# Kernel optimization log

Measured on AMD Instinct MI355X. Metric: run time of the kernel, lower is better.

## Reference

```python
import jax, jax.numpy as jnp
import numpy as np

NUM_HEADS = 8
NUM_POINTS = 4            # sampling points per pillar point
NUM_PILLAR = 4            # points in pillar
SAMPLING_RADIUS = 0.12


def masked_softmax(logits, mask):
    # logits/mask: [B, N, H, P]; softmax over last dim, robust to fully-masked rows
    m = mask.astype(logits.dtype)
    w = jax.nn.softmax(jnp.where(mask, logits, jnp.asarray(-1e9, logits.dtype)), axis=-1) * m
    return w / jnp.clip(jnp.sum(w, axis=-1, keepdims=True), 1e-6)


def grid_sample_bilinear(feat, loc):
    # feat: [G, D, H, W]; loc: [G, Nq, P, 2] normalized to [0,1]
    # matches torch grid_sample(mode='bilinear', padding_mode='zeros', align_corners=False)
    G, D, H, W = feat.shape
    _, Nq, P, _ = loc.shape
    fm = feat.reshape(G, D, H * W).transpose(0, 2, 1)  # [G, HW, D]
    x = loc[..., 0] * W - 0.5
    y = loc[..., 1] * H - 0.5
    x0 = jnp.floor(x)
    y0 = jnp.floor(y)
    wx = x - x0
    wy = y - y0
    out = jnp.zeros((G, Nq * P, D), dtype=feat.dtype)
    corners = [(0, 0, (1 - wx) * (1 - wy)), (1, 0, wx * (1 - wy)),
               (0, 1, (1 - wx) * wy), (1, 1, wx * wy)]
    for dx, dy, w in corners:
        xi = x0 + dx
        yi = y0 + dy
        valid = (xi >= 0) & (xi < W) & (yi >= 0) & (yi < H)
        xc = jnp.clip(xi, 0, W - 1).astype(jnp.int32)
        yc = jnp.clip(yi, 0, H - 1).astype(jnp.int32)
        idx = (yc * W + xc).reshape(G, Nq * P)
        g = jnp.take_along_axis(fm, idx[:, :, None], axis=1)  # [G, Nq*P, D]
        out = out + g * (w * valid.astype(feat.dtype)).reshape(G, Nq * P, 1)
    return out.reshape(G, Nq, P, D)


def setup_inputs() -> dict:
    key = jax.random.key(0)
    ks = jax.random.split(key, 10)
    B, N, C = 1, 10000, 256
    n_cams, Himg, Wimg = 6, 60, 100
    HD = NUM_HEADS * NUM_PILLAR * NUM_POINTS  # 128
    query = jax.random.normal(ks[0], (B, N, C), jnp.float32)
    image_feats = jax.random.normal(ks[1], (B, n_cams, C, Himg, Wimg), jnp.float32)
    reference_points_cam = jax.random.uniform(ks[2], (B, n_cams, N, NUM_PILLAR, 2), jnp.float32)
    bev_mask = jax.random.bernoulli(ks[3], 0.4, (B, n_cams, N, NUM_PILLAR))
    s = 0.02
    offset_W = jax.random.normal(ks[4], (C, HD * 2), jnp.float32) * s
    offset_b = jnp.zeros((HD * 2,), jnp.float32)
    weight_W = jax.random.normal(ks[5], (C, HD), jnp.float32) * s
    weight_b = jnp.zeros((HD,), jnp.float32)
    out_W = jax.random.normal(ks[6], (C, C), jnp.float32) * s
    out_b = jnp.zeros((C,), jnp.float32)
    return {"query": query, "image_feats": image_feats,
            "reference_points_cam": reference_points_cam, "bev_mask": bev_mask,
            "offset_W": offset_W, "offset_b": offset_b,
            "weight_W": weight_W, "weight_b": weight_b,
            "out_W": out_W, "out_b": out_b}


def reference(query, image_feats, reference_points_cam, bev_mask,
              offset_W, offset_b, weight_W, weight_b, out_W, out_b):
    B, N, C = query.shape
    _, n_cams, _, Himg, Wimg = image_feats.shape
    Hh, Pp, Pn = NUM_HEADS, NUM_PILLAR, NUM_POINTS
    P = Pp * Pn
    hd = C // Hh

    offsets = jnp.tanh(query @ offset_W + offset_b) * SAMPLING_RADIUS
    offsets = offsets.reshape(B, N, Hh, Pp, Pn, 2)
    weight_logits = (query @ weight_W + weight_b).reshape(B, N, Hh, P)

    fused = jnp.zeros((B, N, C), query.dtype)
    counts = jnp.zeros((B, N), jnp.int32)
    for cam in range(n_cams):
        ref = reference_points_cam[:, cam]          # [B, N, Pp, 2]
        visible = bev_mask[:, cam]                  # [B, N, Pp]
        loc = ref[:, :, None, :, None, :] + offsets  # [B, N, H, Pp, Pn, 2]
        loc = loc.reshape(B, N, Hh, P, 2)
        vmask = jnp.broadcast_to(visible[:, :, None, :, None], (B, N, Hh, Pp, Pn)).reshape(B, N, Hh, P)
        w = masked_softmax(weight_logits, vmask)    # [B, N, H, P]
        feat = image_feats[:, cam].reshape(B * Hh, hd, Himg, Wimg)
        grid = loc.transpose(0, 2, 1, 3, 4).reshape(B * Hh, N, P, 2)
        samp = grid_sample_bilinear(feat, grid)     # [B*H, N, P, hd]
        samp = samp.reshape(B, Hh, N, P, hd).transpose(0, 2, 1, 3, 4)  # [B, N, H, P, hd]
        cam_out = jnp.sum(samp * w[..., None], axis=3).reshape(B, N, C)
        has_vis = jnp.any(visible, axis=-1)         # [B, N]
        fused = fused + cam_out * has_vis[..., None].astype(cam_out.dtype)
        counts = counts + has_vis.astype(jnp.int32)
    fused = fused / jnp.clip(counts, 1)[..., None].astype(fused.dtype)
    return fused @ out_W + out_b
```

## Files before the change

kernel.cpp:

```cpp
#include <hip/hip_runtime.h>
#include <hip/hip_bf16.h>

#define N_Q   10000
#define N_CAM 6
#define HIMG  60
#define WIMG  100
#define NPIX  6000

typedef __attribute__((ext_vector_type(4))) float f32x4;
typedef __attribute__((ext_vector_type(2))) float f32x2;
typedef __attribute__((ext_vector_type(8))) short bf16x8;

__device__ __forceinline__ unsigned short f2bf(float x) {
  __hip_bfloat16 b = __float2bfloat16(x);
  return *reinterpret_cast<unsigned short*>(&b);
}
__device__ __forceinline__ float bf2f(unsigned short u) {
  return __uint_as_float(((unsigned)u) << 16);
}
__device__ __forceinline__ float bf16lo(unsigned int u) {
  return __uint_as_float(u << 16);
}
__device__ __forceinline__ float bf16hi(unsigned int u) {
  return __uint_as_float(u & 0xffff0000u);
}
__device__ __forceinline__ void pk_fma(f32x2& acc, f32x2 a, f32x2 b) {
  asm("v_pk_fma_f32 %0, %1, %2, %0" : "+v"(acc) : "v"(a), "v"(b));
}
__device__ __forceinline__ void split8(const float* pa, bf16x8& ah, bf16x8& al) {
  const float4 v0 = *reinterpret_cast<const float4*>(pa);
  const float4 v1 = *reinterpret_cast<const float4*>(pa + 4);
  const float v[8] = {v0.x, v0.y, v0.z, v0.w, v1.x, v1.y, v1.z, v1.w};
#pragma unroll
  for (int j = 0; j < 8; ++j) {
    const unsigned short hb = f2bf(v[j]);
    ah[j] = (short)hb;
    al[j] = (short)f2bf(v[j] - bf2f(hb));
  }
}

__global__ __launch_bounds__(256) void wprep_k(
    const float* __restrict__ oW, const float* __restrict__ wW,
    const float* __restrict__ outW,
    unsigned short* __restrict__ oWth,  unsigned short* __restrict__ oWtl,
    unsigned short* __restrict__ wWth,  unsigned short* __restrict__ wWtl,
    unsigned short* __restrict__ outWth,unsigned short* __restrict__ outWtl) {
  const int b = blockIdx.x, k = threadIdx.x;
  float v; unsigned short *dh, *dl; int idx;
  if (b < 256) {
    v = oW[k * 256 + b]; dh = oWth; dl = oWtl; idx = b * 256 + k;
  } else if (b < 384) {
    int nn = b - 256; v = wW[k * 128 + nn]; dh = wWth; dl = wWtl; idx = nn * 256 + k;
  } else {
    int nn = b - 384; v = outW[k * 256 + nn]; dh = outWth; dl = outWtl; idx = nn * 256 + k;
  }
  unsigned short hv = f2bf(v);
  dh[idx] = hv;
  dl[idx] = f2bf(v - bf2f(hv));
}

__device__ __forceinline__ void gemm_bodyA32(
    const float* __restrict__ A,
    const unsigned short* __restrict__ Bh, const unsigned short* __restrict__ Bl,
    const float* __restrict__ bias, float* __restrict__ C,
    int M, int N, int mode, int bm, int bn, int tid) {
  const int l = tid & 63, w = tid >> 6;
  const int wm = w >> 1, wn = w & 1;
  const int lr = l & 15;
  const int lk = (l >> 4) * 8;

  const int am0 = min(bm + wm * 32 + lr, M - 1);
  const int am1 = min(bm + wm * 32 + 16 + lr, M - 1);
  const int bn0 = bn + wn * 32 + lr;
  const int bn1 = bn0 + 16;

  const float* pa0 = A + (size_t)am0 * 256 + lk;
  const float* pa1 = A + (size_t)am1 * 256 + lk;
  const bf16x8* pbh0 = (const bf16x8*)(Bh + (size_t)bn0 * 256 + lk);
  const bf16x8* pbh1 = (const bf16x8*)(Bh + (size_t)bn1 * 256 + lk);
  const bf16x8* pbl0 = (const bf16x8*)(Bl + (size_t)bn0 * 256 + lk);
  const bf16x8* pbl1 = (const bf16x8*)(Bl + (size_t)bn1 * 256 + lk);

  f32x4 acc00 = {}, acc01 = {}, acc10 = {}, acc11 = {};

#pragma unroll
  for (int ks = 0; ks < 8; ++ks) {
    bf16x8 ah0, al0, ah1, al1;
    split8(pa0 + ks * 32, ah0, al0);
    split8(pa1 + ks * 32, ah1, al1);
    bf16x8 bh0 = pbh0[ks * 4], bh1 = pbh1[ks * 4];
    bf16x8 bl0 = pbl0[ks * 4], bl1 = pbl1[ks * 4];
    acc00 = __builtin_amdgcn_mfma_f32_16x16x32_bf16(ah0, bh0, acc00, 0, 0, 0);
    acc00 = __builtin_amdgcn_mfma_f32_16x16x32_bf16(ah0, bl0, acc00, 0, 0, 0);
    acc00 = __builtin_amdgcn_mfma_f32_16x16x32_bf16(al0, bh0, acc00, 0, 0, 0);
    acc01 = __builtin_amdgcn_mfma_f32_16x16x32_bf16(ah0, bh1, acc01, 0, 0, 0);
    acc01 = __builtin_amdgcn_mfma_f32_16x16x32_bf16(ah0, bl1, acc01, 0, 0, 0);
    acc01 = __builtin_amdgcn_mfma_f32_16x16x32_bf16(al0, bh1, acc01, 0, 0, 0);
    acc10 = __builtin_amdgcn_mfma_f32_16x16x32_bf16(ah1, bh0, acc10, 0, 0, 0);
    acc10 = __builtin_amdgcn_mfma_f32_16x16x32_bf16(ah1, bl0, acc10, 0, 0, 0);
    acc10 = __builtin_amdgcn_mfma_f32_16x16x32_bf16(al1, bh0, acc10, 0, 0, 0);
    acc11 = __builtin_amdgcn_mfma_f32_16x16x32_bf16(ah1, bh1, acc11, 0, 0, 0);
    acc11 = __builtin_amdgcn_mfma_f32_16x16x32_bf16(ah1, bl1, acc11, 0, 0, 0);
    acc11 = __builtin_amdgcn_mfma_f32_16x16x32_bf16(al1, bh1, acc11, 0, 0, 0);
  }

  const float bias0 = bias[bn + wn * 32 + lr];
  const float bias1 = bias[bn + wn * 32 + 16 + lr];
  const int row0 = bm + wm * 32 + (l >> 4) * 4;
  const int col0 = bn + wn * 32 + lr;
#pragma unroll
  for (int r = 0; r < 4; ++r) {
    int rowA = row0 + r, rowB = row0 + 16 + r;
    float v00 = acc00[r] + bias0, v01 = acc01[r] + bias1;
    float v10 = acc10[r] + bias0, v11 = acc11[r] + bias1;
    if (mode == 1) {
      v00 = tanhf(v00) * 0.12f; v01 = tanhf(v01) * 0.12f;
      v10 = tanhf(v10) * 0.12f; v11 = tanhf(v11) * 0.12f;
    } else if (mode == 2) {
      v00 = __expf(v00); v01 = __expf(v01);
      v10 = __expf(v10); v11 = __expf(v11);
    }
    if (rowA < M) {
      C[(size_t)rowA * N + col0] = v00;
      C[(size_t)rowA * N + col0 + 16] = v01;
    }
    if (rowB < M) {
      C[(size_t)rowB * N + col0] = v10;
      C[(size_t)rowB * N + col0 + 16] = v11;
    }
  }
}

#define TRANS_BLKS (N_CAM * 94)
#define G12_BLKS   (157 * 6)

__global__ __launch_bounds__(256) void fused_prep_gemm_k(
    const float* __restrict__ in,
    const float* __restrict__ q,
    unsigned short* __restrict__ ftout,
    const unsigned short* __restrict__ B1h, const unsigned short* __restrict__ B1l,
    const float* __restrict__ b1, float* __restrict__ C1,
    const unsigned short* __restrict__ B2h, const unsigned short* __restrict__ B2l,
    const float* __restrict__ b2, float* __restrict__ C2) {
  __shared__ float tile[64][65];
  const int tid = threadIdx.x;
  if (blockIdx.x < TRANS_BLKS) {
    const int cam = blockIdx.x / 94;
    const int px0 = (blockIdx.x % 94) * 64;
    const int lpx = tid & 63;
    const int cg  = tid >> 6;
    const int px  = px0 + lpx;
    const bool pv = px < NPIX;

    for (int c0 = 0; c0 < 256; c0 += 64) {
#pragma unroll
      for (int i = 0; i < 16; ++i) {
        int cc = cg * 16 + i;
        tile[lpx][cc] = pv ? in[(cam * 256 + c0 + cc) * NPIX + px] : 0.f;
      }
      __syncthreads();
      const int wc = tid & 63;
      const int pg = tid >> 6;
#pragma unroll
      for (int i = 0; i < 16; ++i) {
        int lp = pg * 16 + i;
        int gpx = px0 + lp;
        if (gpx < NPIX)
          ftout[(size_t)(cam * NPIX + gpx) * 256 + c0 + wc] = f2bf(tile[lp][wc]);
      }
      __syncthreads();
    }
    return;
  }
  const int b  = blockIdx.x - TRANS_BLKS;
  const int bt = b % 6;
  const int bm = (b / 6) * 64;
  if (bt < 4)
    gemm_bodyA32(q, B1h, B1l, b1, C1, N_Q, 256, 1, bm, bt * 64, tid);
  else
    gemm_bodyA32(q, B2h, B2l, b2, C2, N_Q, 128, 2, bm, (bt - 4) * 64, tid);
}

__global__ __launch_bounds__(256) void sample_cam(
    const unsigned short* __restrict__ ft,
    const float* __restrict__ offs,
    const float* __restrict__ wlog,
    const float* __restrict__ refp,
    const int*   __restrict__ mask,
    unsigned short* __restrict__ partial) {
  const int tid = threadIdx.x;
  const int sub = tid >> 7;
  const int t   = tid & 127;
  const int cam = blockIdx.x / (N_Q / 2);
  const int n   = (blockIdx.x % (N_Q / 2)) * 2 + sub;
  const int h   = t >> 4;
  const int p   = t & 15;
  const int pp  = p >> 2;
  const int c   = (t >> 2) & 3;
  const int ch  = t & 3;

  const int vis = mask[(cam * N_Q + n) * 4 + pp];
  const unsigned long long bal = __ballot(vis != 0);
  if (!(bal & 0x1111ULL)) return;

  __shared__ float spt[2][1216];
  float* lds = spt[sub];
  unsigned int* ldsu = reinterpret_cast<unsigned int*>(lds);

  const float2 off = reinterpret_cast<const float2*>(offs)[n * 128 + t];
  const float E = wlog[n * 128 + t];
  const uint4* ftq2 = reinterpret_cast<const uint4*>(ft)
                      + (size_t)cam * (NPIX * 32) + (unsigned)(h * 4 + ch);

  const int abase = h * 152 + p * 9;
  const int rbase = h * 152;

  float e = vis ? E : 0.f;
  float s = e;
#pragma unroll
  for (int m = 8; m >= 1; m >>= 1)
    s += __shfl_xor(s, m, 16);
  const float wgt = e / fmaxf(s, 1e-6f);

  const float2 ref = reinterpret_cast<const float2*>(refp)[(cam * N_Q + n) * 4 + pp];
  const float x = fmaf(ref.x + off.x, (float)WIMG, -0.5f);
  const float y = fmaf(ref.y + off.y, (float)HIMG, -0.5f);
  const float x0f = floorf(x), y0f = floorf(y);
  const float wx = x - x0f, wy = y - y0f;
  const int x0 = (int)x0f, y0 = (int)y0f;
  const int x1 = x0 + 1, y1 = y0 + 1;
  const float mx0 = (x0 >= 0 && x0 < WIMG) ? 1.f : 0.f;
  const float mx1 = (x1 >= 0 && x1 < WIMG) ? 1.f : 0.f;
  const float my0 = (y0 >= 0 && y0 < HIMG) ? 1.f : 0.f;
  const float my1 = (y1 >= 0 && y1 < HIMG) ? 1.f : 0.f;
  const int xc0 = min(max(x0, 0), WIMG - 1);
  const int xc1 = min(max(x1, 0), WIMG - 1);
  const int yc0 = min(max(y0, 0), HIMG - 1);
  const int yc1 = min(max(y1, 0), HIMG - 1);
  lds[abase + 0] = (1.f - wx) * (1.f - wy) * mx0 * my0 * wgt;
  lds[abase + 1] = wx * (1.f - wy) * mx1 * my0 * wgt;
  lds[abase + 2] = (1.f - wx) * wy * mx0 * my1 * wgt;
  lds[abase + 3] = wx * wy * mx1 * my1 * wgt;
  ldsu[abase + 4] = (unsigned)(yc0 * WIMG + xc0);
  ldsu[abase + 5] = (unsigned)(yc0 * WIMG + xc1);
  ldsu[abase + 6] = (unsigned)(yc1 * WIMG + xc0);
  ldsu[abase + 7] = (unsigned)(yc1 * WIMG + xc1);
  __builtin_amdgcn_wave_barrier();

  f32x2 acc2[4] = {{0.f, 0.f}, {0.f, 0.f}, {0.f, 0.f}, {0.f, 0.f}};
  const bool pv0 = (bal      ) & 1ULL;
  const bool pv1 = (bal >>  4) & 1ULL;
  const bool pv2 = (bal >>  8) & 1ULL;
  const bool pv3 = (bal >> 12) & 1ULL;
  uint4 u0[4], u1[4], u2[4], u3[4];

#define ISSUE(U, P)                                                          \
  if (pv##P) {                                                               \
    _Pragma("unroll")                                                        \
    for (int pn = 0; pn < 4; ++pn) {                                         \
      const unsigned pix = ldsu[rbase + ((P) * 4 + pn) * 9 + 4 + c];         \
      U[pn] = ftq2[pix * 32u];                                               \
    }                                                                        \
  }
  ISSUE(u0, 0) ISSUE(u1, 1) ISSUE(u2, 2) ISSUE(u3, 3)

#define CONSUME(U, P)                                                        \
  if (pv##P) {                                                               \
    _Pragma("unroll")                                                        \
    for (int pn = 0; pn < 4; ++pn) {                                         \
      const float wv = lds[rbase + ((P) * 4 + pn) * 9 + c];                  \
      const f32x2 w2 = {wv, wv};                                             \
      f32x2 a;                                                               \
      a.x = bf16lo(U[pn].x); a.y = __uint_as_float(U[pn].x);                 \
      pk_fma(acc2[0], a, w2);                                                \
      a.x = bf16lo(U[pn].y); a.y = __uint_as_float(U[pn].y);                 \
      pk_fma(acc2[1], a, w2);                                                \
      a.x = bf16lo(U[pn].z); a.y = __uint_as_float(U[pn].z);                 \
      pk_fma(acc2[2], a, w2);                                                \
      a.x = bf16lo(U[pn].w); a.y = __uint_as_float(U[pn].w);                 \
      pk_fma(acc2[3], a, w2);                                                \
    }                                                                        \
  }
  CONSUME(u0, 0) CONSUME(u1, 1) CONSUME(u2, 2) CONSUME(u3, 3)
#undef ISSUE
#undef CONSUME

  float acc[8];
#pragma unroll
  for (int j = 0; j < 4; ++j) { acc[2 * j] = acc2[j].x; acc[2 * j + 1] = acc2[j].y; }
#pragma unroll
  for (int j = 0; j < 8; ++j) acc[j] += __shfl_xor(acc[j], 4);
#pragma unroll
  for (int j = 0; j < 8; ++j) acc[j] += __shfl_xor(acc[j], 8);

  if (c == 0) {
    unsigned w01 = (unsigned)f2bf(acc[0]) | ((unsigned)f2bf(acc[1]) << 16);
    unsigned w23 = (unsigned)f2bf(acc[2]) | ((unsigned)f2bf(acc[3]) << 16);
    unsigned w45 = (unsigned)f2bf(acc[4]) | ((unsigned)f2bf(acc[5]) << 16);
    unsigned w67 = (unsigned)f2bf(acc[6]) | ((unsigned)f2bf(acc[7]) << 16);
    uint4 v = {w01, w23, w45, w67};
    reinterpret_cast<uint4*>(partial)[((size_t)cam * N_Q + n) * 32 + h * 4 + ch] = v;
  }
}

__global__ __launch_bounds__(256) void combine_k(
    const unsigned short* __restrict__ partial,
    const int*   __restrict__ mask,
    unsigned short* __restrict__ fh,
    unsigned short* __restrict__ fl) {
  const int tid  = threadIdx.x;
  const int sub  = tid >> 6;
  const int lane = tid & 63;
  const int n    = blockIdx.x * 4 + sub;

  __shared__ int sv[4][6];
  if (tid < 24) {
    const int qi = tid / 6, cam = tid - qi * 6;
    const int nn = blockIdx.x * 4 + qi;
    const int4 m4 = *reinterpret_cast<const int4*>(&mask[(cam * N_Q + nn) * 4]);
    sv[qi][cam] = (m4.x | m4.y | m4.z | m4.w) ? 1 : 0;
  }
  __syncthreads();

  f32x4 s4 = {0.f, 0.f, 0.f, 0.f};
  int cnt = 0;
#pragma unroll
  for (int cam = 0; cam < N_CAM; ++cam) {
    if (sv[sub][cam]) {
      const uint2 v = reinterpret_cast<const uint2*>(partial)
                          [((size_t)cam * N_Q + n) * 64 + lane];
      s4[0] += bf16lo(v.x); s4[1] += bf16hi(v.x);
      s4[2] += bf16lo(v.y); s4[3] += bf16hi(v.y);
      cnt++;
    }
  }
  const float inv = (cnt > 0) ? (1.f / (float)cnt) : 1.f;
  unsigned short hs[4], ls[4];
#pragma unroll
  for (int j = 0; j < 4; ++j) {
    const float v = s4[j] * inv;
    hs[j] = f2bf(v);
    ls[j] = f2bf(v - bf2f(hs[j]));
  }
  uint2 vh = {(unsigned)hs[0] | ((unsigned)hs[1] << 16),
              (unsigned)hs[2] | ((unsigned)hs[3] << 16)};
  uint2 vl = {(unsigned)ls[0] | ((unsigned)ls[1] << 16),
              (unsigned)ls[2] | ((unsigned)ls[3] << 16)};
  reinterpret_cast<uint2*>(fh)[n * 64 + lane] = vh;
  reinterpret_cast<uint2*>(fl)[n * 64 + lane] = vl;
}

__global__ __launch_bounds__(256) void gemm_out_k(
    const unsigned short* __restrict__ Ah, const unsigned short* __restrict__ Al,
    const unsigned short* __restrict__ Bh, const unsigned short* __restrict__ Bl,
    const float* __restrict__ bias, float* __restrict__ C) {
  const int tid = threadIdx.x;
  const int l = tid & 63, w = tid >> 6;
  const int wm = w >> 1, wn = w & 1;
  const int bm = blockIdx.y * 64, bn = blockIdx.x * 64;
  const int lr = l & 15;
  const int lk = (l >> 4) * 8;
  const int M = N_Q, N = 256;

  const int am0 = min(bm + wm * 32 + lr, M - 1);
  const int am1 = min(bm + wm * 32 + 16 + lr, M - 1);
  const int bn0 = bn + wn * 32 + lr;
  const int bn1 = bn0 + 16;

  const bf16x8* pah0 = (const bf16x8*)(Ah + (size_t)am0 * 256 + lk);
  const bf16x8* pah1 = (const bf16x8*)(Ah + (size_t)am1 * 256 + lk);
  const bf16x8* pal0 = (const bf16x8*)(Al + (size_t)am0 * 256 + lk);
  const bf16x8* pal1 = (const bf16x8*)(Al + (size_t)am1 * 256 + lk);
  const bf16x8* pbh0 = (const bf16x8*)(Bh + (size_t)bn0 * 256 + lk);
  const bf16x8* pbh1 = (const bf16x8*)(Bh + (size_t)bn1 * 256 + lk);
  const bf16x8* pbl0 = (const bf16x8*)(Bl + (size_t)bn0 * 256 + lk);
  const bf16x8* pbl1 = (const bf16x8*)(Bl + (size_t)bn1 * 256 + lk);

  f32x4 acc00 = {}, acc01 = {}, acc10 = {}, acc11 = {};

#pragma unroll
  for (int ks = 0; ks < 8; ++ks) {
    bf16x8 ah0 = pah0[ks * 4], ah1 = pah1[ks * 4];
    bf16x8 al0 = pal0[ks * 4], al1 = pal1[ks * 4];
    bf16x8 bh0 = pbh0[ks * 4], bh1 = pbh1[ks * 4];
    bf16x8 bl0 = pbl0[ks * 4], bl1 = pbl1[ks * 4];
    acc00 = __builtin_amdgcn_mfma_f32_16x16x32_bf16(ah0, bh0, acc00, 0, 0, 0);
    acc00 = __builtin_amdgcn_mfma_f32_16x16x32_bf16(ah0, bl0, acc00, 0, 0, 0);
    acc00 = __builtin_amdgcn_mfma_f32_16x16x32_bf16(al0, bh0, acc00, 0, 0, 0);
    acc01 = __builtin_amdgcn_mfma_f32_16x16x32_bf16(ah0, bh1, acc01, 0, 0, 0);
    acc01 = __builtin_amdgcn_mfma_f32_16x16x32_bf16(ah0, bl1, acc01, 0, 0, 0);
    acc01 = __builtin_amdgcn_mfma_f32_16x16x32_bf16(al0, bh1, acc01, 0, 0, 0);
    acc10 = __builtin_amdgcn_mfma_f32_16x16x32_bf16(ah1, bh0, acc10, 0, 0, 0);
    acc10 = __builtin_amdgcn_mfma_f32_16x16x32_bf16(ah1, bl0, acc10, 0, 0, 0);
    acc10 = __builtin_amdgcn_mfma_f32_16x16x32_bf16(al1, bh0, acc10, 0, 0, 0);
    acc11 = __builtin_amdgcn_mfma_f32_16x16x32_bf16(ah1, bh1, acc11, 0, 0, 0);
    acc11 = __builtin_amdgcn_mfma_f32_16x16x32_bf16(ah1, bl1, acc11, 0, 0, 0);
    acc11 = __builtin_amdgcn_mfma_f32_16x16x32_bf16(al1, bh1, acc11, 0, 0, 0);
  }

  const float bias0 = bias[bn + wn * 32 + lr];
  const float bias1 = bias[bn + wn * 32 + 16 + lr];
  const int row0 = bm + wm * 32 + (l >> 4) * 4;
  const int col0 = bn + wn * 32 + lr;
#pragma unroll
  for (int r = 0; r < 4; ++r) {
    int rowA = row0 + r, rowB = row0 + 16 + r;
    if (rowA < M) {
      C[(size_t)rowA * N + col0] = acc00[r] + bias0;
      C[(size_t)rowA * N + col0 + 16] = acc01[r] + bias1;
    }
    if (rowB < M) {
      C[(size_t)rowB * N + col0] = acc10[r] + bias0;
      C[(size_t)rowB * N + col0 + 16] = acc11[r] + bias1;
    }
  }
}

extern "C" void kernel_launch(void* const* d_in, const int* in_sizes, int n_in,
                              void* d_out, int out_size, void* d_ws, size_t ws_size,
                              hipStream_t stream) {
  const float* query = (const float*)d_in[0];
  const float* feats = (const float*)d_in[1];
  const float* refp  = (const float*)d_in[2];
  const int*   mask  = (const int*)d_in[3];
  const float* oW    = (const float*)d_in[4];
  const float* ob    = (const float*)d_in[5];
  const float* wW    = (const float*)d_in[6];
  const float* wb    = (const float*)d_in[7];
  const float* outW  = (const float*)d_in[8];
  const float* outb  = (const float*)d_in[9];
  float* out = (float*)d_out;

  char* wsb = (char*)d_ws;
  size_t o = 0;
  unsigned short* ft = (unsigned short*)(wsb + o); o += (size_t)N_CAM * NPIX * 256 * 2;
  unsigned short* fh = (unsigned short*)(wsb + o); o += (size_t)N_Q * 256 * 2;
  unsigned short* fl = (unsigned short*)(wsb + o); o += (size_t)N_Q * 256 * 2;
  unsigned short* oWth  = (unsigned short*)(wsb + o); o += 256 * 256 * 2;
  unsigned short* oWtl  = (unsigned short*)(wsb + o); o += 256 * 256 * 2;
  unsigned short* wWth  = (unsigned short*)(wsb + o); o += 128 * 256 * 2;
  unsigned short* wWtl  = (unsigned short*)(wsb + o); o += 128 * 256 * 2;
  unsigned short* outWth = (unsigned short*)(wsb + o); o += 256 * 256 * 2;
  unsigned short* outWtl = (unsigned short*)(wsb + o); o += 256 * 256 * 2;
  float* offs    = (float*)(wsb + o); o += (size_t)N_Q * 256 * 4;
  float* wlog    = (float*)(wsb + o); o += (size_t)N_Q * 128 * 4;
  unsigned short* partial = (unsigned short*)(wsb + o);
  o += (size_t)N_CAM * N_Q * 256 * 2;

  wprep_k<<<640, 256, 0, stream>>>(oW, wW, outW,
                                   oWth, oWtl, wWth, wWtl, outWth, outWtl);

  fused_prep_gemm_k<<<TRANS_BLKS + G12_BLKS, 256, 0, stream>>>(
      feats, query, ft, oWth, oWtl, ob, offs, wWth, wWtl, wb, wlog);

  sample_cam<<<N_CAM * (N_Q / 2), 256, 0, stream>>>(ft, offs, wlog, refp, mask,
                                                    partial);

  combine_k<<<N_Q / 4, 256, 0, stream>>>(partial, mask, fh, fl);

  dim3 g3(4, (N_Q + 63) / 64);
  gemm_out_k<<<g3, 256, 0, stream>>>(fh, fl, outWth, outWtl, outb, out);
}
```

Before: 151.6 us.

## Fuse camera combine into output GEMM with LDS-staged A tiles

Removes the separate combine kernel. The output GEMM now sums the per-camera partials, normalises by the visible-camera count and does the hi/lo bf16 split directly into shared memory for a 64-row tile. Each block covers all 256 output columns: four waves each take 64 columns with a 4x4 fragment grid, and the A operand is read from LDS. This removes the fh/fl round trip through global memory and one kernel launch. In exchange the grid shrinks to about 157 blocks, so occupancy and parallelism drop, and each block carries large LDS and register footprints.

```diff
diff --git a/kernel.cpp b/kernel.cpp
--- a/kernel.cpp
+++ b/kernel.cpp
@@ -303,115 +303,130 @@
   }
 }
 
-__global__ __launch_bounds__(256) void combine_k(
+__global__ __launch_bounds__(256) void gemm_out_k(
     const unsigned short* __restrict__ partial,
     const int*   __restrict__ mask,
-    unsigned short* __restrict__ fh,
-    unsigned short* __restrict__ fl) {
-  const int tid  = threadIdx.x;
-  const int sub  = tid >> 6;
-  const int lane = tid & 63;
-  const int n    = blockIdx.x * 4 + sub;
-
-  __shared__ int sv[4][6];
-  if (tid < 24) {
-    const int qi = tid / 6, cam = tid - qi * 6;
-    const int nn = blockIdx.x * 4 + qi;
-    const int4 m4 = *reinterpret_cast<const int4*>(&mask[(cam * N_Q + nn) * 4]);
-    sv[qi][cam] = (m4.x | m4.y | m4.z | m4.w) ? 1 : 0;
-  }
-  __syncthreads();
-
-  f32x4 s4 = {0.f, 0.f, 0.f, 0.f};
-  int cnt = 0;
-#pragma unroll
-  for (int cam = 0; cam < N_CAM; ++cam) {
-    if (sv[sub][cam]) {
-      const uint2 v = reinterpret_cast<const uint2*>(partial)
-                          [((size_t)cam * N_Q + n) * 64 + lane];
-      s4[0] += bf16lo(v.x); s4[1] += bf16hi(v.x);
-      s4[2] += bf16lo(v.y); s4[3] += bf16hi(v.y);
-      cnt++;
-    }
-  }
-  const float inv = (cnt > 0) ? (1.f / (float)cnt) : 1.f;
-  unsigned short hs[4], ls[4];
-#pragma unroll
-  for (int j = 0; j < 4; ++j) {
-    const float v = s4[j] * inv;
-    hs[j] = f2bf(v);
-    ls[j] = f2bf(v - bf2f(hs[j]));
-  }
-  uint2 vh = {(unsigned)hs[0] | ((unsigned)hs[1] << 16),
-              (unsigned)hs[2] | ((unsigned)hs[3] << 16)};
-  uint2 vl = {(unsigned)ls[0] | ((unsigned)ls[1] << 16),
-              (unsigned)ls[2] | ((unsigned)ls[3] << 16)};
-  reinterpret_cast<uint2*>(fh)[n * 64 + lane] = vh;
-  reinterpret_cast<uint2*>(fl)[n * 64 + lane] = vl;
-}
-
-__global__ __launch_bounds__(256) void gemm_out_k(
-    const unsigned short* __restrict__ Ah, const unsigned short* __restrict__ Al,
     const unsigned short* __restrict__ Bh, const unsigned short* __restrict__ Bl,
     const float* __restrict__ bias, float* __restrict__ C) {
+  __shared__ unsigned short Ahs[64][264];
+  __shared__ unsigned short Als[64][264];
+  __shared__ float    sinv[64];
+  __shared__ unsigned sbits[64];
+
   const int tid = threadIdx.x;
-  const int l = tid & 63, w = tid >> 6;
-  const int wm = w >> 1, wn = w & 1;
-  const int bm = blockIdx.y * 64, bn = blockIdx.x * 64;
+  const int bm  = blockIdx.x * 64;
+
+  if (tid < 64) {
+    const int n = min(bm + tid, N_Q - 1);
+    unsigned bits = 0; int cnt = 0;
+#pragma unroll
+    for (int cam = 0; cam < N_CAM; ++cam) {
+      const int4 m4 = *reinterpret_cast<const int4*>(&mask[(cam * N_Q + n) * 4]);
+      const int any = (m4.x | m4.y | m4.z | m4.w) ? 1 : 0;
+      bits |= (unsigned)any << cam;
+      cnt += any;
+    }
+    sbits[tid] = bits;
+    sinv[tid]  = (cnt > 0) ? (1.f / (float)cnt) : 1.f;
+  }
+  __syncthreads();
+
+  const uint4* pq = reinterpret_cast<const uint4*>(partial);
+#pragma unroll
+  for (int i = 0; i < 8; ++i) {
+    const int u    = tid + i * 256;
+    const int row  = u >> 5;
+    const int slot = u & 31;
+    const int n    = min(bm + row, N_Q - 1);
+    const unsigned bits = sbits[row];
+    const float    inv  = sinv[row];
+    float v[8] = {0.f, 0.f, 0.f, 0.f, 0.f, 0.f, 0.f, 0.f};
+#pragma unroll
+    for (int cam = 0; cam < N_CAM; ++cam) {
+      if ((bits >> cam) & 1u) {
+        const uint4 x = pq[((size_t)cam * N_Q + n) * 32 + slot];
+        v[0] += bf16lo(x.x); v[1] += bf16hi(x.x);
+        v[2] += bf16lo(x.y); v[3] += bf16hi(x.y);
+        v[4] += bf16lo(x.z); v[5] += bf16hi(x.z);
+        v[6] += bf16lo(x.w); v[7] += bf16hi(x.w);
+      }
+    }
+    unsigned short hh[8], ll[8];
+#pragma unroll
+    for (int j = 0; j < 8; ++j) {
+      const float x = v[j] * inv;
+      hh[j] = f2bf(x);
+      ll[j] = f2bf(x - bf2f(hh[j]));
+    }
+    uint4 ph = {(unsigned)hh[0] | ((unsigned)hh[1] << 16),
+                (unsigned)hh[2] | ((unsigned)hh[3] << 16),
+                (unsigned)hh[4] | ((unsigned)hh[5] << 16),
+                (unsigned)hh[6] | ((unsigned)hh[7] << 16)};
+    uint4 pl = {(unsigned)ll[0] | ((unsigned)ll[1] << 16),
+                (unsigned)ll[2] | ((unsigned)ll[3] << 16),
+                (unsigned)ll[4] | ((unsigned)ll[5] << 16),
+                (unsigned)ll[6] | ((unsigned)ll[7] << 16)};
+    *reinterpret_cast<uint4*>(&Ahs[row][slot * 8]) = ph;
+    *reinterpret_cast<uint4*>(&Als[row][slot * 8]) = pl;
+  }
+  __syncthreads();
+
+  const int l  = tid & 63;
+  const int w  = tid >> 6;
   const int lr = l & 15;
   const int lk = (l >> 4) * 8;
-  const int M = N_Q, N = 256;
-
-  const int am0 = min(bm + wm * 32 + lr, M - 1);
-  const int am1 = min(bm + wm * 32 + 16 + lr, M - 1);
-  const int bn0 = bn + wn * 32 + lr;
-  const int bn1 = bn0 + 16;
-
-  const bf16x8* pah0 = (const bf16x8*)(Ah + (size_t)am0 * 256 + lk);
-  const bf16x8* pah1 = (const bf16x8*)(Ah + (size_t)am1 * 256 + lk);
-  const bf16x8* pal0 = (const bf16x8*)(Al + (size_t)am0 * 256 + lk);
-  const bf16x8* pal1 = (const bf16x8*)(Al + (size_t)am1 * 256 + lk);
-  const bf16x8* pbh0 = (const bf16x8*)(Bh + (size_t)bn0 * 256 + lk);
-  const bf16x8* pbh1 = (const bf16x8*)(Bh + (size_t)bn1 * 256 + lk);
-  const bf16x8* pbl0 = (const bf16x8*)(Bl + (size_t)bn0 * 256 + lk);
-  const bf16x8* pbl1 = (const bf16x8*)(Bl + (size_t)bn1 * 256 + lk);
-
-  f32x4 acc00 = {}, acc01 = {}, acc10 = {}, acc11 = {};
+
+  const bf16x8* pbh[4];
+  const bf16x8* pbl[4];
+#pragma unroll
+  for (int cf = 0; cf < 4; ++cf) {
+    const int col = w * 64 + cf * 16 + lr;
+    pbh[cf] = (const bf16x8*)(Bh + (size_t)col * 256 + lk);
+    pbl[cf] = (const bf16x8*)(Bl + (size_t)col * 256 + lk);
+  }
+
+  f32x4 acc[4][4] = {};
 
 #pragma unroll
   for (int ks = 0; ks < 8; ++ks) {
-    bf16x8 ah0 = pah0[ks * 4], ah1 = pah1[ks * 4];
-    bf16x8 al0 = pal0[ks * 4], al1 = pal1[ks * 4];
-    bf16x8 bh0 = pbh0[ks * 4], bh1 = pbh1[ks * 4];
-    bf16x8 bl0 = pbl0[ks * 4], bl1 = pbl1[ks * 4];
-    acc00 = __builtin_amdgcn_mfma_f32_16x16x32_bf16(ah0, bh0, acc00, 0, 0, 0);
-    acc00 = __builtin_amdgcn_mfma_f32_16x16x32_bf16(ah0, bl0, acc00, 0, 0, 0);
-    acc00 = __builtin_amdgcn_mfma_f32_16x16x32_bf16(al0, bh0, acc00, 0, 0, 0);
-    acc01 = __builtin_amdgcn_mfma_f32_16x16x32_bf16(ah0, bh1, acc01, 0, 0, 0);
-    acc01 = __builtin_amdgcn_mfma_f32_16x16x32_bf16(ah0, bl1, acc01, 0, 0, 0);
-    acc01 = __builtin_amdgcn_mfma_f32_16x16x32_bf16(al0, bh1, acc01, 0, 0, 0);
-    acc10 = __builtin_amdgcn_mfma_f32_16x16x32_bf16(ah1, bh0, acc10, 0, 0, 0);
-    acc10 = __builtin_amdgcn_mfma_f32_16x16x32_bf16(ah1, bl0, acc10, 0, 0, 0);
-    acc10 = __builtin_amdgcn_mfma_f32_16x16x32_bf16(al1, bh0, acc10, 0, 0, 0);
-    acc11 = __builtin_amdgcn_mfma_f32_16x16x32_bf16(ah1, bh1, acc11, 0, 0, 0);
-    acc11 = __builtin_amdgcn_mfma_f32_16x16x32_bf16(ah1, bl1, acc11, 0, 0, 0);
-    acc11 = __builtin_amdgcn_mfma_f32_16x16x32_bf16(al1, bh1, acc11, 0, 0, 0);
-  }
-
-  const float bias0 = bias[bn + wn * 32 + lr];
-  const float bias1 = bias[bn + wn * 32 + 16 + lr];
-  const int row0 = bm + wm * 32 + (l >> 4) * 4;
-  const int col0 = bn + wn * 32 + lr;
-#pragma unroll
-  for (int r = 0; r < 4; ++r) {
-    int rowA = row0 + r, rowB = row0 + 16 + r;
-    if (rowA < M) {
-      C[(size_t)rowA * N + col0] = acc00[r] + bias0;
-      C[(size_t)rowA * N + col0 + 16] = acc01[r] + bias1;
-    }
-    if (rowB < M) {
-      C[(size_t)rowB * N + col0] = acc10[r] + bias0;
-      C[(size_t)rowB * N + col0 + 16] = acc11[r] + bias1;
+    bf16x8 ah[4], al[4], bh[4], bl[4];
+#pragma unroll
+    for (int rf = 0; rf < 4; ++rf) {
+      ah[rf] = *reinterpret_cast<const bf16x8*>(&Ahs[rf * 16 + lr][ks * 32 + lk]);
+      al[rf] = *reinterpret_cast<const bf16x8*>(&Als[rf * 16 + lr][ks * 32 + lk]);
+    }
+#pragma unroll
+    for (int cf = 0; cf < 4; ++cf) {
+      bh[cf] = pbh[cf][ks * 4];
+      bl[cf] = pbl[cf][ks * 4];
+    }
+#pragma unroll
+    for (int rf = 0; rf < 4; ++rf)
+#pragma unroll
+      for (int cf = 0; cf < 4; ++cf) {
+        acc[rf][cf] = __builtin_amdgcn_mfma_f32_16x16x32_bf16(ah[rf], bh[cf], acc[rf][cf], 0, 0, 0);
+        acc[rf][cf] = __builtin_amdgcn_mfma_f32_16x16x32_bf16(ah[rf], bl[cf], acc[rf][cf], 0, 0, 0);
+        acc[rf][cf] = __builtin_amdgcn_mfma_f32_16x16x32_bf16(al[rf], bh[cf], acc[rf][cf], 0, 0, 0);
+      }
+  }
+
+  float bias_cf[4];
+#pragma unroll
+  for (int cf = 0; cf < 4; ++cf) bias_cf[cf] = bias[w * 64 + cf * 16 + lr];
+
+#pragma unroll
+  for (int rf = 0; rf < 4; ++rf) {
+    const int row0 = bm + rf * 16 + (l >> 4) * 4;
+#pragma unroll
+    for (int r = 0; r < 4; ++r) {
+      const int row = row0 + r;
+      if (row < N_Q) {
+#pragma unroll
+        for (int cf = 0; cf < 4; ++cf) {
+          const int col = w * 64 + cf * 16 + lr;
+          C[(size_t)row * 256 + col] = acc[rf][cf][r] + bias_cf[cf];
+        }
+      }
     }
   }
 }
@@ -434,8 +449,6 @@
   char* wsb = (char*)d_ws;
   size_t o = 0;
   unsigned short* ft = (unsigned short*)(wsb + o); o += (size_t)N_CAM * NPIX * 256 * 2;
-  unsigned short* fh = (unsigned short*)(wsb + o); o += (size_t)N_Q * 256 * 2;
-  unsigned short* fl = (unsigned short*)(wsb + o); o += (size_t)N_Q * 256 * 2;
   unsigned short* oWth  = (unsigned short*)(wsb + o); o += 256 * 256 * 2;
   unsigned short* oWtl  = (unsigned short*)(wsb + o); o += 256 * 256 * 2;
   unsigned short* wWth  = (unsigned short*)(wsb + o); o += 128 * 256 * 2;
@@ -456,8 +469,6 @@
   sample_cam<<<N_CAM * (N_Q / 2), 256, 0, stream>>>(ft, offs, wlog, refp, mask,
                                                     partial);
 
-  combine_k<<<N_Q / 4, 256, 0, stream>>>(partial, mask, fh, fl);
-
-  dim3 g3(4, (N_Q + 63) / 64);
-  gemm_out_k<<<g3, 256, 0, stream>>>(fh, fl, outWth, outWtl, outb, out);
-}
+  gemm_out_k<<<(N_Q + 63) / 64, 256, 0, stream>>>(partial, mask,
+                                                  outWth, outWtl, outb, out);
+}
```

Result: faster. 147.5 us (-2.7%).
